# Kernel optimization log

Hardware: AMD Instinct MI355X
Metric: run time of the kernel (lower is better)

## Reference

```python
import jax, jax.numpy as jnp
import numpy as np

B, S, D, H = 4, 2048, 1024, 16
DK = D // H
NEG = -1000000000.0


def setup_inputs() -> dict:
    key = jax.random.key(0)
    ks = jax.random.split(key, 12)
    scale = 1.0 / np.sqrt(D)
    inp = {
        "query": jax.random.normal(ks[0], (B, S, D), jnp.float32),
        "key": jax.random.normal(ks[1], (B, S, D), jnp.float32),
        "value": jax.random.normal(ks[2], (B, S, D), jnp.float32),
        "mask": jax.random.randint(ks[3], (B, S, S), 0, 2, jnp.int32),
        "Wq": jax.random.normal(ks[4], (D, D), jnp.float32) * scale,
        "bq": jnp.zeros((D,), jnp.float32),
        "Wk": jax.random.normal(ks[5], (D, D), jnp.float32) * scale,
        "bk": jnp.zeros((D,), jnp.float32),
        "Wv": jax.random.normal(ks[6], (D, D), jnp.float32) * scale,
        "bv": jnp.zeros((D,), jnp.float32),
        "Wo": jax.random.normal(ks[7], (D, D), jnp.float32) * scale,
        "bo": jnp.zeros((D,), jnp.float32),
    }
    return inp


def _split_heads(x):
    # (B, S, D) -> (B, H, S, DK)
    return x.reshape(B, -1, H, DK).transpose(0, 2, 1, 3)


def reference(query, key, value, mask, Wq, bq, Wk, bk, Wv, bv, Wo, bo):
    q = _split_heads(query @ Wq.T + bq)
    k = _split_heads(key @ Wk.T + bk)
    v = _split_heads(value @ Wv.T + bv)
    scores = jnp.einsum('bhqd,bhkd->bhqk', q, k) / jnp.sqrt(jnp.float32(DK))
    scores = jnp.where(mask[:, None, :, :] == 0, NEG, scores)
    p_attn = jax.nn.softmax(scores, axis=-1)
    x = jnp.einsum('bhqk,bhkd->bhqd', p_attn, v)
    x = x.transpose(0, 2, 1, 3).reshape(B, -1, D)
    return x @ Wo.T + bo
```

## Files before the change

### kernel.cpp

```cpp
#include <hip/hip_runtime.h>

#define BDIM 4
#define SDIM 2048
#define DDIM 1024
#define HDIM 16
#define DKDIM 64
#define MDIM (BDIM*SDIM)

typedef __attribute__((ext_vector_type(8))) short bf16x8_t;
typedef __attribute__((ext_vector_type(4))) float f32x4_t;

__device__ __forceinline__ unsigned short f2bf(float f) {
    union { float f; unsigned u; } v; v.f = f;
    unsigned r = v.u + 0x7FFFu + ((v.u >> 16) & 1u);
    return (unsigned short)(r >> 16);
}

__device__ __forceinline__ unsigned pkbf(float a, float b) {
#if defined(__has_builtin) && __has_builtin(__builtin_amdgcn_cvt_pk_bf16_f32)
    auto v = __builtin_amdgcn_cvt_pk_bf16_f32(a, b);
    union { decltype(v) x; unsigned u; } cv; cv.x = v; return cv.u;
#else
    return (unsigned)f2bf(a) | ((unsigned)f2bf(b) << 16);
#endif
}

#if defined(__has_builtin) && __has_builtin(__builtin_amdgcn_exp2f)
#define EXP2F(x) __builtin_amdgcn_exp2f(x)
#else
#define EXP2F(x) __expf((x) * 0.69314718f)
#endif

#define QSCALE 0.18033688011112042f

__device__ __forceinline__ void gl_lds16(const void* g, void* l) {
    __builtin_amdgcn_global_load_lds(
        (const __attribute__((address_space(1))) unsigned int*)g,
        (__attribute__((address_space(3))) unsigned int*)l, 16, 0, 0);
}

__global__ void cvt3(const float* __restrict__ a, const float* __restrict__ b, const float* __restrict__ c,
                     unsigned short* __restrict__ oa, unsigned short* __restrict__ ob, unsigned short* __restrict__ oc,
                     int n4) {
    int i = blockIdx.x * blockDim.x + threadIdx.x;
    const float* s = blockIdx.y == 0 ? a : (blockIdx.y == 1 ? b : c);
    unsigned short* d = blockIdx.y == 0 ? oa : (blockIdx.y == 1 ? ob : oc);
    if (i < n4) {
        float4 v = ((const float4*)s)[i];
        ushort4 o;
        o.x = f2bf(v.x); o.y = f2bf(v.y); o.z = f2bf(v.z); o.w = f2bf(v.w);
        ((ushort4*)d)[i] = o;
    }
}

__global__ void cvt4(const float* __restrict__ a, const float* __restrict__ b,
                     const float* __restrict__ c, const float* __restrict__ e,
                     unsigned short* __restrict__ oa, unsigned short* __restrict__ ob,
                     unsigned short* __restrict__ oc, unsigned short* __restrict__ oe,
                     int n4) {
    int i = blockIdx.x * blockDim.x + threadIdx.x;
    const float* s = blockIdx.y == 0 ? a : (blockIdx.y == 1 ? b : (blockIdx.y == 2 ? c : e));
    unsigned short* d = blockIdx.y == 0 ? oa : (blockIdx.y == 1 ? ob : (blockIdx.y == 2 ? oc : oe));
    if (i < n4) {
        float4 v = ((const float4*)s)[i];
        ushort4 o;
        o.x = f2bf(v.x); o.y = f2bf(v.y); o.z = f2bf(v.z); o.w = f2bf(v.w);
        ((ushort4*)d)[i] = o;
    }
}

__global__ void pack_mask(const int* __restrict__ m, unsigned long long* __restrict__ bits) {
    int g = blockIdx.x * 256 + threadIdx.x;
    unsigned long long bal = __ballot(m[g] != 0);
    if ((threadIdx.x & 63) == 0) bits[g >> 6] = bal;
}

template<int OMODE>
__global__ __launch_bounds__(256) void gemm_nt(
    const unsigned short* __restrict__ A,
    const unsigned short* __restrict__ B,
    const float* __restrict__ bias,
    unsigned short* __restrict__ Cb,
    float* __restrict__ Cf,
    int M, int N, int K, float scale)
{
    __shared__ unsigned short As[128 * 32];
    __shared__ unsigned short Bs[128 * 32];
    const int tid = threadIdx.x;
    const int w = tid >> 6, lane = tid & 63;
    const int wr = w >> 1, wc = w & 1;
    const int quad = lane >> 4, l16 = lane & 15;
    const int bn = blockIdx.x, bm = blockIdx.y;

    const int rl = lane >> 2, cl = (lane & 3) * 8;
    const int c0 = w * 2;
    const unsigned short* gA = A + (size_t)(bm * 128 + c0 * 16 + rl) * K + cl;
    const unsigned short* gB = B + (size_t)(bn * 128 + c0 * 16 + rl) * K + cl;
    unsigned short* lA = As + c0 * 512 + lane * 8;
    unsigned short* lB = Bs + c0 * 512 + lane * 8;

    f32x4_t acc[4][4] = {};

    for (int k0 = 0; k0 < K; k0 += 32) {
        gl_lds16(gA, lA);
        gl_lds16(gA + (size_t)16 * K, lA + 16 * 32);
        gl_lds16(gB, lB);
        gl_lds16(gB + (size_t)16 * K, lB + 16 * 32);
        gA += 32; gB += 32;
        __syncthreads();
        bf16x8_t af[4], bfr[4];
#pragma unroll
        for (int mi = 0; mi < 4; ++mi)
            af[mi] = *(const bf16x8_t*)(As + (wr * 64 + mi * 16 + l16) * 32 + quad * 8);
#pragma unroll
        for (int ni = 0; ni < 4; ++ni)
            bfr[ni] = *(const bf16x8_t*)(Bs + (wc * 64 + ni * 16 + l16) * 32 + quad * 8);
#pragma unroll
        for (int mi = 0; mi < 4; ++mi)
#pragma unroll
            for (int ni = 0; ni < 4; ++ni)
                acc[mi][ni] = __builtin_amdgcn_mfma_f32_16x16x32_bf16(af[mi], bfr[ni], acc[mi][ni], 0, 0, 0);
        __syncthreads();
    }

#pragma unroll
    for (int mi = 0; mi < 4; ++mi) {
#pragma unroll
        for (int ni = 0; ni < 4; ++ni) {
            const int n = bn * 128 + wc * 64 + ni * 16 + l16;
            const int m0 = bm * 128 + wr * 64 + mi * 16 + quad * 4;
            const float bv = bias[n];
            if (OMODE == 1) {
                ushort4 pk;
                pk.x = f2bf((acc[mi][ni][0] + bv) * scale);
                pk.y = f2bf((acc[mi][ni][1] + bv) * scale);
                pk.z = f2bf((acc[mi][ni][2] + bv) * scale);
                pk.w = f2bf((acc[mi][ni][3] + bv) * scale);
                *(ushort4*)(Cb + (size_t)n * M + m0) = pk;
            } else {
#pragma unroll
                for (int r = 0; r < 4; ++r) {
                    const float v = (acc[mi][ni][r] + bv) * scale;
                    if (OMODE == 0) Cb[(size_t)(m0 + r) * N + n] = f2bf(v);
                    else            Cf[(size_t)(m0 + r) * N + n] = v;
                }
            }
        }
    }
}

__global__ __launch_bounds__(256) void attn_kernel(
    const unsigned short* __restrict__ Qp,
    const unsigned short* __restrict__ Kp,
    const unsigned short* __restrict__ Vt,
    const unsigned long long* __restrict__ mbits,
    unsigned short* __restrict__ Xa)
{
    __shared__ unsigned short Ks[2 * 64 * 32];
    __shared__ unsigned short Vs[2 * 64 * 32];
    __shared__ __align__(16) float Pf[4][2][2][16][36];

    const int tid = threadIdx.x, w = tid >> 6, lane = tid & 63;
    const int quad = lane >> 4, l16 = lane & 15;
    const int bx = blockIdx.x;
    const int h = bx & 15, qt = (bx >> 4) & 15, b = bx >> 8;
    const int q0 = qt * 128;
    const int rl = lane >> 2, cl = (lane & 3) * 8;

#pragma unroll
    for (int i = 0; i < 4; ++i) {
        const int cc = w * 4 + i;
        const int row = b * SDIM + q0 + (cc & 7) * 16 + rl;
        const int col = h * 64 + (cc >> 3) * 32 + cl;
        unsigned short* dst = (cc < 8 ? Ks + cc * 512 : Vs + (cc - 8) * 512) + lane * 8;
        gl_lds16(Qp + (size_t)row * DDIM + col, dst);
    }
    __syncthreads();
    bf16x8_t aq[2][2];
#pragma unroll
    for (int g = 0; g < 2; ++g) {
        aq[g][0] = *(const bf16x8_t*)(Ks + (w * 2 + g) * 512 + l16 * 32 + quad * 8);
        aq[g][1] = *(const bf16x8_t*)(Vs + (w * 2 + g) * 512 + l16 * 32 + quad * 8);
    }

    const unsigned long long* mp =
        mbits + (size_t)(b * SDIM + q0 + w * 32 + quad * 4) * 32;

    f32x4_t o[2][4] = {};
    f32x4_t o4[2] = {};
    union { unsigned u[4]; bf16x8_t v; } ones;
    ones.u[0] = ones.u[1] = ones.u[2] = ones.u[3] = 0x3F803F80u;

    for (int kt = 0; kt < SDIM / 64; ++kt) {
        __syncthreads();
#pragma unroll
        for (int i = 0; i < 2; ++i) {
            const int cc = w * 2 + i;
            const int rowk = b * SDIM + kt * 64 + (cc & 3) * 16 + rl;
            const int colk = h * 64 + (cc >> 2) * 32 + cl;
            gl_lds16(Kp + (size_t)rowk * DDIM + colk, Ks + cc * 512 + lane * 8);
            const int rowv = h * 64 + (cc & 3) * 16 + rl;
            const int colv = b * SDIM + kt * 64 + (cc >> 2) * 32 + cl;
            gl_lds16(Vt + (size_t)rowv * MDIM + colv, Vs + cc * 512 + lane * 8);
        }
        __syncthreads();

        unsigned long long mb[2][4];
#pragma unroll
        for (int g = 0; g < 2; ++g)
#pragma unroll
            for (int r = 0; r < 4; ++r) mb[g][r] = mp[g * 512 + r * 32 + kt];

        f32x4_t sf[2][4] = {};
#pragma unroll
        for (int kk = 0; kk < 2; ++kk) {
#pragma unroll
            for (int ni = 0; ni < 4; ++ni) {
                const bf16x8_t bk = *(const bf16x8_t*)(Ks + kk * 2048 + (ni * 16 + l16) * 32 + quad * 8);
                sf[0][ni] = __builtin_amdgcn_mfma_f32_16x16x32_bf16(aq[0][kk], bk, sf[0][ni], 0, 0, 0);
                sf[1][ni] = __builtin_amdgcn_mfma_f32_16x16x32_bf16(aq[1][kk], bk, sf[1][ni], 0, 0, 0);
            }
        }

#pragma unroll
        for (int g = 0; g < 2; ++g) {
#pragma unroll
            for (int r = 0; r < 4; ++r) {
                const unsigned long long sh = mb[g][r] >> l16;
                const unsigned mlo = (unsigned)sh;
                const unsigned mhi = (unsigned)(sh >> 32);
                const int row = quad * 4 + r;
                const float t0 = (mlo & 1u)         ? sf[g][0][r] : -INFINITY;
                const float t1 = ((mlo >> 16) & 1u) ? sf[g][1][r] : -INFINITY;
                const float t2 = (mhi & 1u)         ? sf[g][2][r] : -INFINITY;
                const float t3 = ((mhi >> 16) & 1u) ? sf[g][3][r] : -INFINITY;
                Pf[w][g][0][row][l16]      = EXP2F(t0);
                Pf[w][g][0][row][16 + l16] = EXP2F(t1);
                Pf[w][g][1][row][l16]      = EXP2F(t2);
                Pf[w][g][1][row][16 + l16] = EXP2F(t3);
            }
        }

#pragma unroll
        for (int kk = 0; kk < 2; ++kk) {
            bf16x8_t bvf[4];
#pragma unroll
            for (int ni = 0; ni < 4; ++ni)
                bvf[ni] = *(const bf16x8_t*)(Vs + kk * 2048 + (ni * 16 + l16) * 32 + quad * 8);
#pragma unroll
            for (int g = 0; g < 2; ++g) {
                const float* pr = &Pf[w][g][kk][l16][quad * 8];
                const float4 pa = *(const float4*)pr;
                const float4 pb = *(const float4*)(pr + 4);
                union { unsigned u[4]; bf16x8_t v; } fu;
                fu.u[0] = pkbf(pa.x, pa.y);
                fu.u[1] = pkbf(pa.z, pa.w);
                fu.u[2] = pkbf(pb.x, pb.y);
                fu.u[3] = pkbf(pb.z, pb.w);
#pragma unroll
                for (int ni = 0; ni < 4; ++ni)
                    o[g][ni] = __builtin_amdgcn_mfma_f32_16x16x32_bf16(fu.v, bvf[ni], o[g][ni], 0, 0, 0);
                o4[g] = __builtin_amdgcn_mfma_f32_16x16x32_bf16(fu.v, ones.v, o4[g], 0, 0, 0);
            }
        }
    }

#pragma unroll
    for (int g = 0; g < 2; ++g) {
        float rcp[4];
#pragma unroll
        for (int r = 0; r < 4; ++r) rcp[r] = 1.0f / o4[g][r];
#pragma unroll
        for (int ni = 0; ni < 4; ++ni)
#pragma unroll
            for (int r = 0; r < 4; ++r) {
                const int qg = q0 + w * 32 + g * 16 + quad * 4 + r;
                const int cg = h * 64 + ni * 16 + l16;
                Xa[((size_t)b * SDIM + qg) * DDIM + cg] = f2bf(o[g][ni][r] * rcp[r]);
            }
    }
}

extern "C" void kernel_launch(void* const* d_in, const int* in_sizes, int n_in,
                              void* d_out, int out_size, void* d_ws, size_t ws_size,
                              hipStream_t stream)
{
    const float* query = (const float*)d_in[0];
    const float* key   = (const float*)d_in[1];
    const float* value = (const float*)d_in[2];
    const int*   mask  = (const int*)d_in[3];
    const float* Wq = (const float*)d_in[4];  const float* bq = (const float*)d_in[5];
    const float* Wk = (const float*)d_in[6];  const float* bk = (const float*)d_in[7];
    const float* Wv = (const float*)d_in[8];  const float* bv = (const float*)d_in[9];
    const float* Wo = (const float*)d_in[10]; const float* bo = (const float*)d_in[11];

    const size_t MD = (size_t)MDIM * DDIM;
    const size_t DD = (size_t)DDIM * DDIM;

    unsigned short* qb  = (unsigned short*)d_ws;
    unsigned short* kb  = qb + MD;
    unsigned short* vb  = kb + MD;
    unsigned short* wqb = vb + MD;
    unsigned short* wkb = wqb + DD;
    unsigned short* wvb = wkb + DD;
    unsigned short* wob = wvb + DD;
    unsigned short* Qp  = wob + DD;
    unsigned short* Kp  = Qp + MD;
    unsigned short* Vt  = Kp + MD;
    unsigned short* Xa  = Vt + MD;
    unsigned long long* mbits = (unsigned long long*)qb;

    {
        const int n4m = (int)(MD / 4), n4d = (int)(DD / 4);
        dim3 g3((n4m + 255) / 256, 3), g4((n4d + 255) / 256, 4);
        cvt3<<<g3, 256, 0, stream>>>(query, key, value, qb, kb, vb, n4m);
        cvt4<<<g4, 256, 0, stream>>>(Wq, Wk, Wv, Wo, wqb, wkb, wvb, wob, n4d);
    }

    dim3 gg(DDIM / 128, MDIM / 128);
    gemm_nt<0><<<gg, 256, 0, stream>>>(qb, wqb, bq, Qp, nullptr, MDIM, DDIM, DDIM, QSCALE);
    gemm_nt<0><<<gg, 256, 0, stream>>>(kb, wkb, bk, Kp, nullptr, MDIM, DDIM, DDIM, 1.0f);
    gemm_nt<1><<<gg, 256, 0, stream>>>(vb, wvb, bv, Vt, nullptr, MDIM, DDIM, DDIM, 1.0f);

    pack_mask<<<(BDIM * SDIM * SDIM) / 256, 256, 0, stream>>>(mask, mbits);

    attn_kernel<<<BDIM * HDIM * (SDIM / 128), 256, 0, stream>>>(Qp, Kp, Vt, mbits, Xa);

    gemm_nt<2><<<gg, 256, 0, stream>>>(Xa, wob, bo, nullptr, (float*)d_out, MDIM, DDIM, DDIM, 1.0f);
}
```

Measured before the change: 499.7 us.

## Swizzle LDS tiles and preload transposed additive bf16 mask into score accumulators

Applies an XOR swizzle to the LDS column layout in the GEMM and attention kernels to reduce bank conflicts on fragment reads. Replaces the packed bitmask with a transposed bf16 additive mask (0 or a large negative), loaded directly as the initial value of the QK^T accumulators, which removes per-element select logic. This raises mask memory traffic considerably, since a 16x larger mask is re-read for every head.

```diff
diff --git a/kernel.cpp b/kernel.cpp
--- a/kernel.cpp
+++ b/kernel.cpp
@@ -23,6 +23,13 @@
 #else
     return (unsigned)f2bf(a) | ((unsigned)f2bf(b) << 16);
 #endif
+}
+
+__device__ __forceinline__ float bflo(unsigned u) {
+    union { unsigned u; float f; } v; v.u = u << 16; return v.f;
+}
+__device__ __forceinline__ float bfhi(unsigned u) {
+    union { unsigned u; float f; } v; v.u = u & 0xFFFF0000u; return v.f;
 }
 
 #if defined(__has_builtin) && __has_builtin(__builtin_amdgcn_exp2f)
@@ -69,10 +76,25 @@
     }
 }
 
-__global__ void pack_mask(const int* __restrict__ m, unsigned long long* __restrict__ bits) {
-    int g = blockIdx.x * 256 + threadIdx.x;
-    unsigned long long bal = __ballot(m[g] != 0);
-    if ((threadIdx.x & 63) == 0) bits[g >> 6] = bal;
+__global__ __launch_bounds__(256) void mask_t(const int* __restrict__ m, unsigned short* __restrict__ Madd) {
+    __shared__ unsigned short T[64][68];
+    const int t = threadIdx.x;
+    const int k0 = blockIdx.x * 64, q0 = blockIdx.y * 64, b = blockIdx.z;
+    const int lane = t & 63, wv = t >> 6;
+#pragma unroll
+    for (int i = 0; i < 16; ++i) {
+        const int q = wv * 16 + i;
+        const int v = m[((size_t)b * SDIM + q0 + q) * SDIM + k0 + lane];
+        T[lane][q] = v ? (unsigned short)0 : (unsigned short)0xCE6Eu;
+    }
+    __syncthreads();
+    const int k = t >> 2, qc = t & 3;
+#pragma unroll
+    for (int j = 0; j < 4; ++j) {
+        const int q = qc * 16 + j * 4;
+        ushort4 o = *(const ushort4*)&T[k][q];
+        *(ushort4*)&Madd[((size_t)b * SDIM + k0 + k) * SDIM + q0 + q] = o;
+    }
 }
 
 template<int OMODE>
@@ -92,7 +114,9 @@
     const int quad = lane >> 4, l16 = lane & 15;
     const int bn = blockIdx.x, bm = blockIdx.y;
 
-    const int rl = lane >> 2, cl = (lane & 3) * 8;
+    const int rl = lane >> 2;
+    const int cl = (((lane & 3) ^ ((rl >> 1) & 3)) * 8);
+    const int sw = (l16 >> 1) & 3;
     const int c0 = w * 2;
     const unsigned short* gA = A + (size_t)(bm * 128 + c0 * 16 + rl) * K + cl;
     const unsigned short* gB = B + (size_t)(bn * 128 + c0 * 16 + rl) * K + cl;
@@ -111,10 +135,10 @@
         bf16x8_t af[4], bfr[4];
 #pragma unroll
         for (int mi = 0; mi < 4; ++mi)
-            af[mi] = *(const bf16x8_t*)(As + (wr * 64 + mi * 16 + l16) * 32 + quad * 8);
+            af[mi] = *(const bf16x8_t*)(As + (wr * 64 + mi * 16 + l16) * 32 + (quad ^ sw) * 8);
 #pragma unroll
         for (int ni = 0; ni < 4; ++ni)
-            bfr[ni] = *(const bf16x8_t*)(Bs + (wc * 64 + ni * 16 + l16) * 32 + quad * 8);
+            bfr[ni] = *(const bf16x8_t*)(Bs + (wc * 64 + ni * 16 + l16) * 32 + (quad ^ sw) * 8);
 #pragma unroll
         for (int mi = 0; mi < 4; ++mi)
 #pragma unroll
@@ -153,7 +177,7 @@
     const unsigned short* __restrict__ Qp,
     const unsigned short* __restrict__ Kp,
     const unsigned short* __restrict__ Vt,
-    const unsigned long long* __restrict__ mbits,
+    const unsigned short* __restrict__ Madd,
     unsigned short* __restrict__ Xa)
 {
     __shared__ unsigned short Ks[2 * 64 * 32];
@@ -165,7 +189,9 @@
     const int bx = blockIdx.x;
     const int h = bx & 15, qt = (bx >> 4) & 15, b = bx >> 8;
     const int q0 = qt * 128;
-    const int rl = lane >> 2, cl = (lane & 3) * 8;
+    const int rl = lane >> 2;
+    const int cl = (((lane & 3) ^ ((rl >> 1) & 3)) * 8);
+    const int sw = (l16 >> 1) & 3;
 
 #pragma unroll
     for (int i = 0; i < 4; ++i) {
@@ -179,12 +205,12 @@
     bf16x8_t aq[2][2];
 #pragma unroll
     for (int g = 0; g < 2; ++g) {
-        aq[g][0] = *(const bf16x8_t*)(Ks + (w * 2 + g) * 512 + l16 * 32 + quad * 8);
-        aq[g][1] = *(const bf16x8_t*)(Vs + (w * 2 + g) * 512 + l16 * 32 + quad * 8);
-    }
-
-    const unsigned long long* mp =
-        mbits + (size_t)(b * SDIM + q0 + w * 32 + quad * 4) * 32;
+        aq[g][0] = *(const bf16x8_t*)(Ks + (w * 2 + g) * 512 + l16 * 32 + (quad ^ sw) * 8);
+        aq[g][1] = *(const bf16x8_t*)(Vs + (w * 2 + g) * 512 + l16 * 32 + (quad ^ sw) * 8);
+    }
+
+    const unsigned short* mbase =
+        Madd + (size_t)b * SDIM * SDIM + q0 + w * 32 + quad * 4;
 
     f32x4_t o[2][4] = {};
     f32x4_t o4[2] = {};
@@ -205,18 +231,25 @@
         }
         __syncthreads();
 
-        unsigned long long mb[2][4];
-#pragma unroll
-        for (int g = 0; g < 2; ++g)
-#pragma unroll
-            for (int r = 0; r < 4; ++r) mb[g][r] = mp[g * 512 + r * 32 + kt];
-
-        f32x4_t sf[2][4] = {};
+        f32x4_t sf[2][4];
+#pragma unroll
+        for (int ni = 0; ni < 4; ++ni) {
+            const unsigned short* mrow = mbase + (size_t)(kt * 64 + ni * 16 + l16) * SDIM;
+#pragma unroll
+            for (int g = 0; g < 2; ++g) {
+                const uint2 md = *(const uint2*)(mrow + g * 16);
+                sf[g][ni][0] = bflo(md.x);
+                sf[g][ni][1] = bfhi(md.x);
+                sf[g][ni][2] = bflo(md.y);
+                sf[g][ni][3] = bfhi(md.y);
+            }
+        }
+
 #pragma unroll
         for (int kk = 0; kk < 2; ++kk) {
 #pragma unroll
             for (int ni = 0; ni < 4; ++ni) {
-                const bf16x8_t bk = *(const bf16x8_t*)(Ks + kk * 2048 + (ni * 16 + l16) * 32 + quad * 8);
+                const bf16x8_t bk = *(const bf16x8_t*)(Ks + kk * 2048 + (ni * 16 + l16) * 32 + (quad ^ sw) * 8);
                 sf[0][ni] = __builtin_amdgcn_mfma_f32_16x16x32_bf16(aq[0][kk], bk, sf[0][ni], 0, 0, 0);
                 sf[1][ni] = __builtin_amdgcn_mfma_f32_16x16x32_bf16(aq[1][kk], bk, sf[1][ni], 0, 0, 0);
             }
@@ -226,18 +259,11 @@
         for (int g = 0; g < 2; ++g) {
 #pragma unroll
             for (int r = 0; r < 4; ++r) {
-                const unsigned long long sh = mb[g][r] >> l16;
-                const unsigned mlo = (unsigned)sh;
-                const unsigned mhi = (unsigned)(sh >> 32);
                 const int row = quad * 4 + r;
-                const float t0 = (mlo & 1u)         ? sf[g][0][r] : -INFINITY;
-                const float t1 = ((mlo >> 16) & 1u) ? sf[g][1][r] : -INFINITY;
-                const float t2 = (mhi & 1u)         ? sf[g][2][r] : -INFINITY;
-                const float t3 = ((mhi >> 16) & 1u) ? sf[g][3][r] : -INFINITY;
-                Pf[w][g][0][row][l16]      = EXP2F(t0);
-                Pf[w][g][0][row][16 + l16] = EXP2F(t1);
-                Pf[w][g][1][row][l16]      = EXP2F(t2);
-                Pf[w][g][1][row][16 + l16] = EXP2F(t3);
+                Pf[w][g][0][row][l16]      = EXP2F(sf[g][0][r]);
+                Pf[w][g][0][row][16 + l16] = EXP2F(sf[g][1][r]);
+                Pf[w][g][1][row][l16]      = EXP2F(sf[g][2][r]);
+                Pf[w][g][1][row][16 + l16] = EXP2F(sf[g][3][r]);
             }
         }
 
@@ -246,7 +272,7 @@
             bf16x8_t bvf[4];
 #pragma unroll
             for (int ni = 0; ni < 4; ++ni)
-                bvf[ni] = *(const bf16x8_t*)(Vs + kk * 2048 + (ni * 16 + l16) * 32 + quad * 8);
+                bvf[ni] = *(const bf16x8_t*)(Vs + kk * 2048 + (ni * 16 + l16) * 32 + (quad ^ sw) * 8);
 #pragma unroll
             for (int g = 0; g < 2; ++g) {
                 const float* pr = &Pf[w][g][kk][l16][quad * 8];
@@ -308,7 +334,7 @@
     unsigned short* Kp  = Qp + MD;
     unsigned short* Vt  = Kp + MD;
     unsigned short* Xa  = Vt + MD;
-    unsigned long long* mbits = (unsigned long long*)qb;
+    unsigned short* Madd = qb;
 
     {
         const int n4m = (int)(MD / 4), n4d = (int)(DD / 4);
@@ -322,9 +348,9 @@
     gemm_nt<0><<<gg, 256, 0, stream>>>(kb, wkb, bk, Kp, nullptr, MDIM, DDIM, DDIM, 1.0f);
     gemm_nt<1><<<gg, 256, 0, stream>>>(vb, wvb, bv, Vt, nullptr, MDIM, DDIM, DDIM, 1.0f);
 
-    pack_mask<<<(BDIM * SDIM * SDIM) / 256, 256, 0, stream>>>(mask, mbits);
-
-    attn_kernel<<<BDIM * HDIM * (SDIM / 128), 256, 0, stream>>>(Qp, Kp, Vt, mbits, Xa);
+    mask_t<<<dim3(SDIM / 64, SDIM / 64, BDIM), 256, 0, stream>>>(mask, Madd);
+
+    attn_kernel<<<BDIM * HDIM * (SDIM / 128), 256, 0, stream>>>(Qp, Kp, Vt, Madd, Xa);
 
     gemm_nt<2><<<gg, 256, 0, stream>>>(Xa, wob, bo, nullptr, (float*)d_out, MDIM, DDIM, DDIM, 1.0f);
 }
```

New measurement: 557.3 us. 11.5% more time.

## Swizzle LDS tiles, keep softmax probabilities in registers via transposed MFMA

Applied to the files above, without the earlier changes.

Applies an XOR swizzle to the LDS tile layout in both the GEMM and attention kernels to cut bank conflicts on the bf16x8 fragment reads. The attention kernel swaps the MFMA operand order so scores come out transposed, which lets the exp'd probabilities be packed to bf16 in registers and redistributed with lane shuffles instead of going through an fp32 LDS staging buffer. Mask bits are loaded as one 64-bit word per row instead of eight per tile. The output is staged through LDS for 16-byte coalesced stores. Masked scores now use -1e9 instead of -inf, and the shuffle logic and transposed layout are intricate enough to carry a correctness risk.

```diff
diff --git a/kernel.cpp b/kernel.cpp
--- a/kernel.cpp
+++ b/kernel.cpp
@@ -92,7 +92,9 @@
     const int quad = lane >> 4, l16 = lane & 15;
     const int bn = blockIdx.x, bm = blockIdx.y;
 
-    const int rl = lane >> 2, cl = (lane & 3) * 8;
+    const int rl = lane >> 2;
+    const int cl = (((lane & 3) ^ ((rl >> 1) & 3)) * 8);
+    const int sw = (l16 >> 1) & 3;
     const int c0 = w * 2;
     const unsigned short* gA = A + (size_t)(bm * 128 + c0 * 16 + rl) * K + cl;
     const unsigned short* gB = B + (size_t)(bn * 128 + c0 * 16 + rl) * K + cl;
@@ -111,10 +113,10 @@
         bf16x8_t af[4], bfr[4];
 #pragma unroll
         for (int mi = 0; mi < 4; ++mi)
-            af[mi] = *(const bf16x8_t*)(As + (wr * 64 + mi * 16 + l16) * 32 + quad * 8);
+            af[mi] = *(const bf16x8_t*)(As + (wr * 64 + mi * 16 + l16) * 32 + (quad ^ sw) * 8);
 #pragma unroll
         for (int ni = 0; ni < 4; ++ni)
-            bfr[ni] = *(const bf16x8_t*)(Bs + (wc * 64 + ni * 16 + l16) * 32 + quad * 8);
+            bfr[ni] = *(const bf16x8_t*)(Bs + (wc * 64 + ni * 16 + l16) * 32 + (quad ^ sw) * 8);
 #pragma unroll
         for (int mi = 0; mi < 4; ++mi)
 #pragma unroll
@@ -156,35 +158,40 @@
     const unsigned long long* __restrict__ mbits,
     unsigned short* __restrict__ Xa)
 {
-    __shared__ unsigned short Ks[2 * 64 * 32];
-    __shared__ unsigned short Vs[2 * 64 * 32];
-    __shared__ __align__(16) float Pf[4][2][2][16][36];
+    __shared__ unsigned short SMEM[8192];
+    unsigned short* const Ks = SMEM;
+    unsigned short* const Vs = SMEM + 4096;
 
     const int tid = threadIdx.x, w = tid >> 6, lane = tid & 63;
     const int quad = lane >> 4, l16 = lane & 15;
     const int bx = blockIdx.x;
     const int h = bx & 15, qt = (bx >> 4) & 15, b = bx >> 8;
     const int q0 = qt * 128;
-    const int rl = lane >> 2, cl = (lane & 3) * 8;
+    const int rl = lane >> 2;
+    const int cl = (((lane & 3) ^ ((rl >> 1) & 3)) * 8);
+    const int sw = (l16 >> 1) & 3;
+    const bool hi16 = (lane & 16) != 0;
+    const bool hi32 = (lane & 32) != 0;
+    const int idxA = (2 * (quad & 1) + (quad >> 1)) * 16 + l16;
+    const int idxC = idxA ^ 16;
 
 #pragma unroll
     for (int i = 0; i < 4; ++i) {
         const int cc = w * 4 + i;
         const int row = b * SDIM + q0 + (cc & 7) * 16 + rl;
         const int col = h * 64 + (cc >> 3) * 32 + cl;
-        unsigned short* dst = (cc < 8 ? Ks + cc * 512 : Vs + (cc - 8) * 512) + lane * 8;
-        gl_lds16(Qp + (size_t)row * DDIM + col, dst);
+        gl_lds16(Qp + (size_t)row * DDIM + col, SMEM + cc * 512 + lane * 8);
     }
     __syncthreads();
     bf16x8_t aq[2][2];
 #pragma unroll
-    for (int g = 0; g < 2; ++g) {
-        aq[g][0] = *(const bf16x8_t*)(Ks + (w * 2 + g) * 512 + l16 * 32 + quad * 8);
-        aq[g][1] = *(const bf16x8_t*)(Vs + (w * 2 + g) * 512 + l16 * 32 + quad * 8);
-    }
-
-    const unsigned long long* mp =
-        mbits + (size_t)(b * SDIM + q0 + w * 32 + quad * 4) * 32;
+    for (int g = 0; g < 2; ++g)
+#pragma unroll
+        for (int kk = 0; kk < 2; ++kk)
+            aq[g][kk] = *(const bf16x8_t*)(SMEM + (kk * 8 + w * 2 + g) * 512 + l16 * 32 + (quad ^ sw) * 8);
+
+    const unsigned long long* mq0 = mbits + (size_t)(b * SDIM + q0 + w * 32 + l16) * 32;
+    const unsigned long long* mq1 = mq0 + (size_t)16 * 32;
 
     f32x4_t o[2][4] = {};
     f32x4_t o4[2] = {};
@@ -205,79 +212,90 @@
         }
         __syncthreads();
 
-        unsigned long long mb[2][4];
-#pragma unroll
-        for (int g = 0; g < 2; ++g)
-#pragma unroll
-            for (int r = 0; r < 4; ++r) mb[g][r] = mp[g * 512 + r * 32 + kt];
+        const unsigned long long sh0 = mq0[kt] >> (quad * 4);
+        const unsigned long long sh1 = mq1[kt] >> (quad * 4);
 
         f32x4_t sf[2][4] = {};
 #pragma unroll
         for (int kk = 0; kk < 2; ++kk) {
 #pragma unroll
             for (int ni = 0; ni < 4; ++ni) {
-                const bf16x8_t bk = *(const bf16x8_t*)(Ks + kk * 2048 + (ni * 16 + l16) * 32 + quad * 8);
-                sf[0][ni] = __builtin_amdgcn_mfma_f32_16x16x32_bf16(aq[0][kk], bk, sf[0][ni], 0, 0, 0);
-                sf[1][ni] = __builtin_amdgcn_mfma_f32_16x16x32_bf16(aq[1][kk], bk, sf[1][ni], 0, 0, 0);
+                const bf16x8_t ak = *(const bf16x8_t*)(Ks + kk * 2048 + (ni * 16 + l16) * 32 + (quad ^ sw) * 8);
+                sf[0][ni] = __builtin_amdgcn_mfma_f32_16x16x32_bf16(ak, aq[0][kk], sf[0][ni], 0, 0, 0);
+                sf[1][ni] = __builtin_amdgcn_mfma_f32_16x16x32_bf16(ak, aq[1][kk], sf[1][ni], 0, 0, 0);
             }
         }
 
+        unsigned P[2][4][2];
 #pragma unroll
         for (int g = 0; g < 2; ++g) {
-#pragma unroll
-            for (int r = 0; r < 4; ++r) {
-                const unsigned long long sh = mb[g][r] >> l16;
-                const unsigned mlo = (unsigned)sh;
-                const unsigned mhi = (unsigned)(sh >> 32);
-                const int row = quad * 4 + r;
-                const float t0 = (mlo & 1u)         ? sf[g][0][r] : -INFINITY;
-                const float t1 = ((mlo >> 16) & 1u) ? sf[g][1][r] : -INFINITY;
-                const float t2 = (mhi & 1u)         ? sf[g][2][r] : -INFINITY;
-                const float t3 = ((mhi >> 16) & 1u) ? sf[g][3][r] : -INFINITY;
-                Pf[w][g][0][row][l16]      = EXP2F(t0);
-                Pf[w][g][0][row][16 + l16] = EXP2F(t1);
-                Pf[w][g][1][row][l16]      = EXP2F(t2);
-                Pf[w][g][1][row][16 + l16] = EXP2F(t3);
+            const unsigned long long s = g ? sh1 : sh0;
+            const unsigned mlo = (unsigned)s, mhi = (unsigned)(s >> 32);
+#pragma unroll
+            for (int ni = 0; ni < 4; ++ni) {
+                const unsigned msel = (ni < 2) ? mlo : mhi;
+                const int shf = (ni & 1) * 16;
+                float p[4];
+#pragma unroll
+                for (int r = 0; r < 4; ++r) {
+                    const bool on = (msel >> (shf + r)) & 1u;
+                    p[r] = EXP2F(on ? sf[g][ni][r] : -1.0e9f);
+                }
+                P[g][ni][0] = pkbf(p[0], p[1]);
+                P[g][ni][1] = pkbf(p[2], p[3]);
             }
         }
 
 #pragma unroll
-        for (int kk = 0; kk < 2; ++kk) {
-            bf16x8_t bvf[4];
+        for (int kk2 = 0; kk2 < 2; ++kk2) {
+            bf16x8_t va[4];
 #pragma unroll
             for (int ni = 0; ni < 4; ++ni)
-                bvf[ni] = *(const bf16x8_t*)(Vs + kk * 2048 + (ni * 16 + l16) * 32 + quad * 8);
+                va[ni] = *(const bf16x8_t*)(Vs + kk2 * 2048 + (ni * 16 + l16) * 32 + (quad ^ sw) * 8);
 #pragma unroll
             for (int g = 0; g < 2; ++g) {
-                const float* pr = &Pf[w][g][kk][l16][quad * 8];
-                const float4 pa = *(const float4*)pr;
-                const float4 pb = *(const float4*)(pr + 4);
-                union { unsigned u[4]; bf16x8_t v; } fu;
-                fu.u[0] = pkbf(pa.x, pa.y);
-                fu.u[1] = pkbf(pa.z, pa.w);
-                fu.u[2] = pkbf(pb.x, pb.y);
-                fu.u[3] = pkbf(pb.z, pb.w);
+                const unsigned Pa = P[g][kk2 * 2][0], Pb = P[g][kk2 * 2][1];
+                const unsigned Pc = P[g][kk2 * 2 + 1][0], Pd = P[g][kk2 * 2 + 1][1];
+                const int RA = hi16 ? (int)Pc : (int)Pa;
+                const int RB = hi16 ? (int)Pd : (int)Pb;
+                const int RC = hi16 ? (int)Pa : (int)Pc;
+                const int RD = hi16 ? (int)Pb : (int)Pd;
+                const int Av = __shfl(RA, idxA, 64);
+                const int Bv = __shfl(RB, idxA, 64);
+                const int Cv = __shfl(RC, idxC, 64);
+                const int Dv = __shfl(RD, idxC, 64);
+                union { unsigned u[4]; bf16x8_t v; } pf;
+                pf.u[0] = (unsigned)(hi32 ? Cv : Av);
+                pf.u[1] = (unsigned)(hi32 ? Dv : Bv);
+                pf.u[2] = (unsigned)(hi32 ? Av : Cv);
+                pf.u[3] = (unsigned)(hi32 ? Bv : Dv);
 #pragma unroll
                 for (int ni = 0; ni < 4; ++ni)
-                    o[g][ni] = __builtin_amdgcn_mfma_f32_16x16x32_bf16(fu.v, bvf[ni], o[g][ni], 0, 0, 0);
-                o4[g] = __builtin_amdgcn_mfma_f32_16x16x32_bf16(fu.v, ones.v, o4[g], 0, 0, 0);
+                    o[g][ni] = __builtin_amdgcn_mfma_f32_16x16x32_bf16(va[ni], pf.v, o[g][ni], 0, 0, 0);
+                o4[g] = __builtin_amdgcn_mfma_f32_16x16x32_bf16(ones.v, pf.v, o4[g], 0, 0, 0);
             }
         }
     }
 
+    __syncthreads();
+    unsigned short* T = SMEM + w * 1152;
 #pragma unroll
     for (int g = 0; g < 2; ++g) {
-        float rcp[4];
-#pragma unroll
-        for (int r = 0; r < 4; ++r) rcp[r] = 1.0f / o4[g][r];
-#pragma unroll
-        for (int ni = 0; ni < 4; ++ni)
-#pragma unroll
-            for (int r = 0; r < 4; ++r) {
-                const int qg = q0 + w * 32 + g * 16 + quad * 4 + r;
-                const int cg = h * 64 + ni * 16 + l16;
-                Xa[((size_t)b * SDIM + qg) * DDIM + cg] = f2bf(o[g][ni][r] * rcp[r]);
-            }
+        const float rcp = 1.0f / o4[g][0];
+#pragma unroll
+        for (int ni = 0; ni < 4; ++ni) {
+            uint2 pk;
+            pk.x = pkbf(o[g][ni][0] * rcp, o[g][ni][1] * rcp);
+            pk.y = pkbf(o[g][ni][2] * rcp, o[g][ni][3] * rcp);
+            *(uint2*)&T[l16 * 72 + ni * 16 + quad * 4] = pk;
+        }
+        const int qrow = q0 + w * 32 + g * 16 + (lane >> 2);
+        const int dkc = (lane & 3) * 16;
+        const bf16x8_t r0 = *(const bf16x8_t*)&T[(lane >> 2) * 72 + dkc];
+        const bf16x8_t r1 = *(const bf16x8_t*)&T[(lane >> 2) * 72 + dkc + 8];
+        unsigned short* dst = Xa + (size_t)(b * SDIM + qrow) * DDIM + h * 64 + dkc;
+        *(bf16x8_t*)dst = r0;
+        *(bf16x8_t*)(dst + 8) = r1;
     }
 }
 
```

Result: no change. 490.2 us (-1.9%).
